# Performance work log

Measured on AMD Instinct MI355X. Metric: run time of the kernel, lower is better.

Reference implementation:

```python
import jax, jax.numpy as jnp
import numpy as np

B, N, E, H = 2, 4096, 512, 8
D = E // H  # head size


def setup_inputs() -> dict:
    key = jax.random.key(0)
    ks = jax.random.split(key, 11)
    s = 1.0 / np.sqrt(E)
    inp = {
        'q': jax.random.normal(ks[0], (B, N, E), jnp.float32),
        'k': jax.random.normal(ks[1], (B, N, E), jnp.float32),
        'v': jax.random.normal(ks[2], (B, N, E), jnp.float32),
        'Wq': jax.random.uniform(ks[3], (E, E), jnp.float32, -s, s),
        'bq': jax.random.uniform(ks[4], (E,), jnp.float32, -s, s),
        'Wk': jax.random.uniform(ks[5], (E, E), jnp.float32, -s, s),
        'bk': jax.random.uniform(ks[6], (E,), jnp.float32, -s, s),
        'Wv': jax.random.uniform(ks[7], (E, E), jnp.float32, -s, s),
        'bv': jax.random.uniform(ks[8], (E,), jnp.float32, -s, s),
        'Wo': jax.random.uniform(ks[9], (E, E), jnp.float32, -s, s),
        'bo': jax.random.uniform(ks[10], (E,), jnp.float32, -s, s),
    }
    return inp


def reference(q, k, v, Wq, bq, Wk, bk, Wv, bv, Wo, bo):
    # Linear projections (torch Linear: x @ W.T + b)
    qp = (q @ Wq.T + bq).reshape(B, N, H, D).transpose(0, 2, 1, 3)  # [B,H,N,D]
    kp = (k @ Wk.T + bk).reshape(B, N, H, D).transpose(0, 2, 1, 3)
    vp = (v @ Wv.T + bv).reshape(B, N, H, D).transpose(0, 2, 1, 3)
    scores = jnp.einsum('bhnd,bhmd->bhnm', qp, kp) / jnp.sqrt(jnp.float32(D))
    attn = jax.nn.softmax(scores, axis=-1)
    out = jnp.einsum('bhnm,bhmd->bhnd', attn, vp)  # [B,H,N,D]
    out = out.transpose(0, 2, 1, 3).reshape(B, N, E)
    return out @ Wo.T + bo
```

## Files before the change

### kernel.cpp

```cpp
#include <hip/hip_runtime.h>
#include <hip/hip_bf16.h>
#include <cstddef>


typedef __bf16 bf16_t;
typedef __bf16 bf16x8 __attribute__((ext_vector_type(8)));
typedef __bf16 bf16x4 __attribute__((ext_vector_type(4)));
typedef float  f32x4  __attribute__((ext_vector_type(4)));

#define MFMA_BF16 __builtin_amdgcn_mfma_f32_16x16x32_bf16

static __device__ __forceinline__ bf16x8 cvt2(const float4& a, const float4& b) {
  return bf16x8{(bf16_t)a.x,(bf16_t)a.y,(bf16_t)a.z,(bf16_t)a.w,
                (bf16_t)b.x,(bf16_t)b.y,(bf16_t)b.z,(bf16_t)b.w};
}

__global__ void __launch_bounds__(256, 2)
qkv_proj(const float* __restrict__ q, const float* __restrict__ k,
         const float* __restrict__ v,
         const float* __restrict__ Wq, const float* __restrict__ bq,
         const float* __restrict__ Wk, const float* __restrict__ bk,
         const float* __restrict__ Wv, const float* __restrict__ bv,
         bf16_t* __restrict__ Qp, bf16_t* __restrict__ Kp,
         bf16_t* __restrict__ Vt, float qscale)
{
  __shared__ __align__(16) bf16_t As[2][128 * 72];
  __shared__ __align__(16) bf16_t Bs[2][64 * 72];
  const int l     = blockIdx.x;
  const int slice = l >> 9;
  const int inner = l & 511;
  const int mtile = ((inner >> 6) << 3) | (inner & 7);
  const int ntile = (inner >> 3) & 7;
  const int tid   = threadIdx.x;
  const int w     = tid >> 6;
  const int lane  = tid & 63;
  const int lr    = lane & 15;
  const int quad  = lane >> 4;
  const int wm    = w & 1;
  const int wn    = w >> 1;
  const int xrow  = tid >> 1, xcol = (tid & 1) << 5;
  const int wrow  = tid >> 2, wcol = (tid & 3) << 4;

  const float* Xf   = (slice == 0) ? q  : (slice == 1) ? k  : v;
  const float* W    = (slice == 0) ? Wq : (slice == 1) ? Wk : Wv;
  const float* bias = (slice == 0) ? bq : (slice == 1) ? bk : bv;
  const float scale = (slice == 0) ? qscale : 1.0f;

  float bvv[2];
#pragma unroll
  for (int ci = 0; ci < 2; ++ci) bvv[ci] = bias[ntile * 64 + wn * 32 + ci * 16 + lr];

  f32x4 acc[4][2] = {};
  float4 xa[8], wa[4];

#pragma unroll
  for (int j = 0; j < 4; ++j) {
    const float* p = Xf + (size_t)(mtile * 128 + xrow) * 512 + xcol + j * 8;
    xa[2*j]   = *(const float4*)p;
    xa[2*j+1] = *(const float4*)(p + 4);
  }
#pragma unroll
  for (int j = 0; j < 2; ++j) {
    const float* pw = W + (size_t)(ntile * 64 + wrow) * 512 + wcol + j * 8;
    wa[2*j]   = *(const float4*)pw;
    wa[2*j+1] = *(const float4*)(pw + 4);
  }
#pragma unroll
  for (int j = 0; j < 4; ++j)
    *(bf16x8*)(&As[0][xrow * 72 + xcol + j * 8]) = cvt2(xa[2*j], xa[2*j+1]);
#pragma unroll
  for (int j = 0; j < 2; ++j)
    *(bf16x8*)(&Bs[0][wrow * 72 + wcol + j * 8]) = cvt2(wa[2*j], wa[2*j+1]);
  __syncthreads();

  for (int it = 0; it < 8; ++it) {
    const int cur = it & 1, nxt = cur ^ 1;
    if (it != 7) {
      const int k0 = (it + 1) << 6;
#pragma unroll
      for (int j = 0; j < 4; ++j) {
        const float* p = Xf + (size_t)(mtile * 128 + xrow) * 512 + k0 + xcol + j * 8;
        xa[2*j]   = *(const float4*)p;
        xa[2*j+1] = *(const float4*)(p + 4);
      }
#pragma unroll
      for (int j = 0; j < 2; ++j) {
        const float* pw = W + (size_t)(ntile * 64 + wrow) * 512 + k0 + wcol + j * 8;
        wa[2*j]   = *(const float4*)pw;
        wa[2*j+1] = *(const float4*)(pw + 4);
      }
    }
    bf16x8 af[4][2], bfr[2][2];
#pragma unroll
    for (int mi = 0; mi < 4; ++mi)
#pragma unroll
      for (int kh = 0; kh < 2; ++kh)
        af[mi][kh] = *(const bf16x8*)(&As[cur][(wm * 64 + mi * 16 + lr) * 72 + (kh * 4 + quad) * 8]);
#pragma unroll
    for (int ci = 0; ci < 2; ++ci)
#pragma unroll
      for (int kh = 0; kh < 2; ++kh)
        bfr[ci][kh] = *(const bf16x8*)(&Bs[cur][(wn * 32 + ci * 16 + lr) * 72 + (kh * 4 + quad) * 8]);
#pragma unroll
    for (int mi = 0; mi < 4; ++mi)
#pragma unroll
      for (int ci = 0; ci < 2; ++ci) {
        acc[mi][ci] = MFMA_BF16(af[mi][0], bfr[ci][0], acc[mi][ci], 0, 0, 0);
        acc[mi][ci] = MFMA_BF16(af[mi][1], bfr[ci][1], acc[mi][ci], 0, 0, 0);
      }
    if (it != 7) {
#pragma unroll
      for (int j = 0; j < 4; ++j)
        *(bf16x8*)(&As[nxt][xrow * 72 + xcol + j * 8]) = cvt2(xa[2*j], xa[2*j+1]);
#pragma unroll
      for (int j = 0; j < 2; ++j)
        *(bf16x8*)(&Bs[nxt][wrow * 72 + wcol + j * 8]) = cvt2(wa[2*j], wa[2*j+1]);
    }
    __syncthreads();
  }

  bf16_t* outQK = (slice == 0) ? Qp : Kp;
#pragma unroll
  for (int mi = 0; mi < 4; ++mi) {
    const int gm0 = mtile * 128 + wm * 64 + mi * 16 + quad * 4;
#pragma unroll
    for (int ci = 0; ci < 2; ++ci) {
      const int gc = ntile * 64 + wn * 32 + ci * 16 + lr;
      const int h = gc >> 6, dd = gc & 63;
      if (slice < 2) {
#pragma unroll
        for (int r = 0; r < 4; ++r) {
          const int gm = gm0 + r;
          const int b = gm >> 12, n = gm & 4095;
          outQK[(size_t)((b * 8 + h) * 4096 + n) * 64 + dd] =
              (bf16_t)((acc[mi][ci][r] + bvv[ci]) * scale);
        }
      } else {
        const int b = gm0 >> 12, n0 = gm0 & 4095;
        bf16x4 pk;
#pragma unroll
        for (int r = 0; r < 4; ++r) pk[r] = (bf16_t)(acc[mi][ci][r] + bvv[ci]);
        *(bf16x4*)(Vt + (size_t)((b * 8 + h) * 64 + dd) * 4096 + n0) = pk;
      }
    }
  }
}

__global__ void __launch_bounds__(256, 2)
o_proj(const bf16_t* __restrict__ Xb, const float* __restrict__ W,
       const float* __restrict__ bias, float* __restrict__ out)
{
  __shared__ __align__(16) bf16_t As[2][128 * 72];
  __shared__ __align__(16) bf16_t Bs[2][64 * 72];
  const int l     = blockIdx.x;
  const int mtile = ((l >> 6) << 3) | (l & 7);
  const int ntile = (l >> 3) & 7;
  const int tid   = threadIdx.x;
  const int w     = tid >> 6;
  const int lane  = tid & 63;
  const int lr    = lane & 15;
  const int quad  = lane >> 4;
  const int wm    = w & 1;
  const int wn    = w >> 1;
  const int xrow  = tid >> 1, xcol = (tid & 1) << 5;
  const int wrow  = tid >> 2, wcol = (tid & 3) << 4;

  float bvv[2];
#pragma unroll
  for (int ci = 0; ci < 2; ++ci) bvv[ci] = bias[ntile * 64 + wn * 32 + ci * 16 + lr];

  f32x4 acc[4][2] = {};
  float4 wa[4];
  bf16x8 xb[4];

#pragma unroll
  for (int j = 0; j < 4; ++j)
    xb[j] = *(const bf16x8*)(Xb + (size_t)(mtile * 128 + xrow) * 512 + xcol + j * 8);
#pragma unroll
  for (int j = 0; j < 2; ++j) {
    const float* pw = W + (size_t)(ntile * 64 + wrow) * 512 + wcol + j * 8;
    wa[2*j]   = *(const float4*)pw;
    wa[2*j+1] = *(const float4*)(pw + 4);
  }
#pragma unroll
  for (int j = 0; j < 4; ++j)
    *(bf16x8*)(&As[0][xrow * 72 + xcol + j * 8]) = xb[j];
#pragma unroll
  for (int j = 0; j < 2; ++j)
    *(bf16x8*)(&Bs[0][wrow * 72 + wcol + j * 8]) = cvt2(wa[2*j], wa[2*j+1]);
  __syncthreads();

  for (int it = 0; it < 8; ++it) {
    const int cur = it & 1, nxt = cur ^ 1;
    if (it != 7) {
      const int k0 = (it + 1) << 6;
#pragma unroll
      for (int j = 0; j < 4; ++j)
        xb[j] = *(const bf16x8*)(Xb + (size_t)(mtile * 128 + xrow) * 512 + k0 + xcol + j * 8);
#pragma unroll
      for (int j = 0; j < 2; ++j) {
        const float* pw = W + (size_t)(ntile * 64 + wrow) * 512 + k0 + wcol + j * 8;
        wa[2*j]   = *(const float4*)pw;
        wa[2*j+1] = *(const float4*)(pw + 4);
      }
    }
    bf16x8 af[4][2], bfr[2][2];
#pragma unroll
    for (int mi = 0; mi < 4; ++mi)
#pragma unroll
      for (int kh = 0; kh < 2; ++kh)
        af[mi][kh] = *(const bf16x8*)(&As[cur][(wm * 64 + mi * 16 + lr) * 72 + (kh * 4 + quad) * 8]);
#pragma unroll
    for (int ci = 0; ci < 2; ++ci)
#pragma unroll
      for (int kh = 0; kh < 2; ++kh)
        bfr[ci][kh] = *(const bf16x8*)(&Bs[cur][(wn * 32 + ci * 16 + lr) * 72 + (kh * 4 + quad) * 8]);
#pragma unroll
    for (int mi = 0; mi < 4; ++mi)
#pragma unroll
      for (int ci = 0; ci < 2; ++ci) {
        acc[mi][ci] = MFMA_BF16(af[mi][0], bfr[ci][0], acc[mi][ci], 0, 0, 0);
        acc[mi][ci] = MFMA_BF16(af[mi][1], bfr[ci][1], acc[mi][ci], 0, 0, 0);
      }
    if (it != 7) {
#pragma unroll
      for (int j = 0; j < 4; ++j)
        *(bf16x8*)(&As[nxt][xrow * 72 + xcol + j * 8]) = xb[j];
#pragma unroll
      for (int j = 0; j < 2; ++j)
        *(bf16x8*)(&Bs[nxt][wrow * 72 + wcol + j * 8]) = cvt2(wa[2*j], wa[2*j+1]);
    }
    __syncthreads();
  }

#pragma unroll
  for (int mi = 0; mi < 4; ++mi) {
    const int gm0 = mtile * 128 + wm * 64 + mi * 16 + quad * 4;
#pragma unroll
    for (int ci = 0; ci < 2; ++ci) {
      const int gc = ntile * 64 + wn * 32 + ci * 16 + lr;
#pragma unroll
      for (int r = 0; r < 4; ++r)
        out[(size_t)(gm0 + r) * 512 + gc] = acc[mi][ci][r] + bvv[ci];
    }
  }
}

__global__ void __launch_bounds__(256, 2)
flash_attn(const bf16_t* __restrict__ Qp, const bf16_t* __restrict__ Kp,
           const bf16_t* __restrict__ Vt, bf16_t* __restrict__ Oc)
{
  __shared__ __align__(16) bf16_t Klds[2][64 * 72];
  __shared__ __align__(16) bf16_t Vlds[2][64 * 72];
  __shared__ __align__(16) bf16_t Pl[4][32 * 72];

  const int tid  = threadIdx.x;
  const int w    = tid >> 6;
  const int lane = tid & 63, lr = lane & 15, quad = lane >> 4;
  const int bh   = blockIdx.x;
  const int qt0  = blockIdx.y * 128 + w * 32;

  const bf16_t* Qh = Qp + (size_t)bh * 4096 * 64;
  const bf16_t* Kh = Kp + (size_t)bh * 4096 * 64;
  const bf16_t* Vh = Vt + (size_t)bh * 64 * 4096;

  const int srow = w * 16 + (lane >> 2);
  const int scol = (lane & 3) << 4;

  bf16x8 qf[2][2];
#pragma unroll
  for (int qi = 0; qi < 2; ++qi)
#pragma unroll
    for (int kh = 0; kh < 2; ++kh)
      qf[qi][kh] = *(const bf16x8*)(Qh + (size_t)(qt0 + qi * 16 + lr) * 64 + kh * 32 + quad * 8);

  bf16x8 kst[2], vst[2];
#pragma unroll
  for (int j = 0; j < 2; ++j) {
    kst[j] = *(const bf16x8*)(Kh + (size_t)srow * 64 + scol + j * 8);
    vst[j] = *(const bf16x8*)(Vh + (size_t)srow * 4096 + scol + j * 8);
  }
#pragma unroll
  for (int j = 0; j < 2; ++j) {
    *(bf16x8*)(&Klds[0][srow * 72 + scol + j * 8]) = kst[j];
    *(bf16x8*)(&Vlds[0][srow * 72 + scol + j * 8]) = vst[j];
  }
  __syncthreads();

  f32x4 acc[2][4] = {};
  float lsum[2] = {0.f, 0.f};
  const f32x4 zero = {0.f, 0.f, 0.f, 0.f};
  bf16_t* Pw = &Pl[w][0];

  for (int it = 0; it < 64; ++it) {
    const int cur = it & 1, nxt = cur ^ 1;

    if (it != 63) {
      const int kvn = (it + 1) << 6;
#pragma unroll
      for (int j = 0; j < 2; ++j) {
        kst[j] = *(const bf16x8*)(Kh + (size_t)(kvn + srow) * 64 + scol + j * 8);
        vst[j] = *(const bf16x8*)(Vh + (size_t)srow * 4096 + kvn + scol + j * 8);
      }
    }

    bf16x8 kf[4][2];
#pragma unroll
    for (int mt = 0; mt < 4; ++mt)
#pragma unroll
      for (int kh = 0; kh < 2; ++kh)
        kf[mt][kh] = *(const bf16x8*)(&Klds[cur][(mt * 16 + lr) * 72 + (kh * 4 + quad) * 8]);
    bf16x8 vf[4][2];
#pragma unroll
    for (int t = 0; t < 4; ++t)
#pragma unroll
      for (int kvh = 0; kvh < 2; ++kvh)
        vf[t][kvh] = *(const bf16x8*)(&Vlds[cur][(t * 16 + lr) * 72 + (kvh * 4 + quad) * 8]);

    f32x4 sT[4][2];
#pragma unroll
    for (int mt = 0; mt < 4; ++mt)
#pragma unroll
      for (int qi = 0; qi < 2; ++qi) {
        sT[mt][qi] = MFMA_BF16(kf[mt][0], qf[qi][0], zero, 0, 0, 0);
        sT[mt][qi] = MFMA_BF16(kf[mt][1], qf[qi][1], sT[mt][qi], 0, 0, 0);
      }

#pragma unroll
    for (int mt = 0; mt < 4; ++mt)
#pragma unroll
      for (int qi = 0; qi < 2; ++qi) {
        float p0 = __builtin_amdgcn_exp2f(sT[mt][qi][0]);
        float p1 = __builtin_amdgcn_exp2f(sT[mt][qi][1]);
        float p2 = __builtin_amdgcn_exp2f(sT[mt][qi][2]);
        float p3 = __builtin_amdgcn_exp2f(sT[mt][qi][3]);
        lsum[qi] += (p0 + p1) + (p2 + p3);
        bf16x4 pk = {(bf16_t)p0, (bf16_t)p1, (bf16_t)p2, (bf16_t)p3};
        *(bf16x4*)(Pw + (qi * 16 + lr) * 72 + mt * 16 + quad * 4) = pk;
      }

    bf16x8 pa[2][2];
#pragma unroll
    for (int qi = 0; qi < 2; ++qi)
#pragma unroll
      for (int kvh = 0; kvh < 2; ++kvh)
        pa[qi][kvh] = *(const bf16x8*)(Pw + (qi * 16 + lr) * 72 + kvh * 32 + quad * 8);

#pragma unroll
    for (int t = 0; t < 4; ++t)
#pragma unroll
      for (int qi = 0; qi < 2; ++qi) {
        acc[qi][t] = MFMA_BF16(pa[qi][0], vf[t][0], acc[qi][t], 0, 0, 0);
        acc[qi][t] = MFMA_BF16(pa[qi][1], vf[t][1], acc[qi][t], 0, 0, 0);
      }

    if (it != 63) {
#pragma unroll
      for (int j = 0; j < 2; ++j) {
        *(bf16x8*)(&Klds[nxt][srow * 72 + scol + j * 8]) = kst[j];
        *(bf16x8*)(&Vlds[nxt][srow * 72 + scol + j * 8]) = vst[j];
      }
    }
    __syncthreads();
  }

#pragma unroll
  for (int qi = 0; qi < 2; ++qi) {
    lsum[qi] += __shfl_xor(lsum[qi], 16);
    lsum[qi] += __shfl_xor(lsum[qi], 32);
  }

  const int b = bh >> 3, h = bh & 7;
  bf16_t* Ob = Oc + (size_t)b * 4096 * 512 + h * 64;
#pragma unroll
  for (int qi = 0; qi < 2; ++qi) {
    float inv[4];
#pragma unroll
    for (int r = 0; r < 4; ++r)
      inv[r] = 1.0f / __shfl(lsum[qi], quad * 4 + r);
#pragma unroll
    for (int t = 0; t < 4; ++t)
#pragma unroll
      for (int r = 0; r < 4; ++r) {
        const int n = qt0 + qi * 16 + quad * 4 + r;
        Ob[(size_t)n * 512 + t * 16 + lr] = (bf16_t)(acc[qi][t][r] * inv[r]);
      }
  }
}

extern "C" void kernel_launch(void* const* d_in, const int* in_sizes, int n_in,
                              void* d_out, int out_size, void* d_ws, size_t ws_size,
                              hipStream_t stream)
{
  const float* q  = (const float*)d_in[0];
  const float* k  = (const float*)d_in[1];
  const float* v  = (const float*)d_in[2];
  const float* Wq = (const float*)d_in[3];
  const float* bq = (const float*)d_in[4];
  const float* Wk = (const float*)d_in[5];
  const float* bk = (const float*)d_in[6];
  const float* Wv = (const float*)d_in[7];
  const float* bv = (const float*)d_in[8];
  const float* Wo = (const float*)d_in[9];
  const float* bo = (const float*)d_in[10];

  const size_t HEAD_ELEMS = (size_t)2 * 8 * 4096 * 64;
  bf16_t* Qp = (bf16_t*)d_ws;
  bf16_t* Kp = Qp + HEAD_ELEMS;
  bf16_t* Vt = Kp + HEAD_ELEMS;
  bf16_t* Oc = Vt + HEAD_ELEMS;

  const float qscale = 0.125f * 1.44269504f;

  qkv_proj<<<dim3(1536), 256, 0, stream>>>(q, k, v, Wq, bq, Wk, bk, Wv, bv,
                                           Qp, Kp, Vt, qscale);
  flash_attn<<<dim3(16, 32), 256, 0, stream>>>(Qp, Kp, Vt, Oc);
  o_proj<<<dim3(512), 256, 0, stream>>>(Oc, Wo, bo, (float*)d_out);
}
```

Measured before the change: 268.6 us.

## Widen projection GEMM tiles to 128x128 and pass P via register permlane swaps

The QKV and output projection GEMMs move from 128x64 to 128x128 output tiles, which halves the block count and doubles each block's MFMA work per LDS load, so fp32 X tiles are re-read and converted less often. In flash attention, the exp'd probability tile is no longer written to and read back from a per-wave LDS buffer. It is instead packed with v_cvt_pk_bf16_f32 and reshuffled into the MFMA A-operand layout with v_permlane32/16_swap. The larger tiles raise register and LDS use and give fewer blocks for occupancy. The permlane path relies on a specific lane-mapping assumption that must match the MFMA layout.

New measurement: 260.6 us. 1.03x faster.

```diff
diff --git a/kernel.cpp b/kernel.cpp
--- a/kernel.cpp
+++ b/kernel.cpp
@@ -1,6 +1,7 @@
 #include <hip/hip_runtime.h>
 #include <hip/hip_bf16.h>
 #include <cstddef>
+#include <cstdint>
 
 
 typedef __bf16 bf16_t;
@@ -13,6 +14,12 @@
 static __device__ __forceinline__ bf16x8 cvt2(const float4& a, const float4& b) {
   return bf16x8{(bf16_t)a.x,(bf16_t)a.y,(bf16_t)a.z,(bf16_t)a.w,
                 (bf16_t)b.x,(bf16_t)b.y,(bf16_t)b.z,(bf16_t)b.w};
+}
+
+static __device__ __forceinline__ uint32_t pk2(float a, float b) {
+  uint32_t r;
+  asm("v_cvt_pk_bf16_f32 %0, %1, %2" : "=v"(r) : "v"(a), "v"(b));
+  return r;
 }
 
 __global__ void __launch_bounds__(256, 2)
@@ -25,12 +32,12 @@
          bf16_t* __restrict__ Vt, float qscale)
 {
   __shared__ __align__(16) bf16_t As[2][128 * 72];
-  __shared__ __align__(16) bf16_t Bs[2][64 * 72];
+  __shared__ __align__(16) bf16_t Bs[2][128 * 72];
   const int l     = blockIdx.x;
-  const int slice = l >> 9;
-  const int inner = l & 511;
-  const int mtile = ((inner >> 6) << 3) | (inner & 7);
-  const int ntile = (inner >> 3) & 7;
+  const int slice = l >> 8;
+  const int inner = l & 255;
+  const int mtile = ((inner >> 5) << 3) | (inner & 7);
+  const int ntile = (inner >> 3) & 3;
   const int tid   = threadIdx.x;
   const int w     = tid >> 6;
   const int lane  = tid & 63;
@@ -39,38 +46,33 @@
   const int wm    = w & 1;
   const int wn    = w >> 1;
   const int xrow  = tid >> 1, xcol = (tid & 1) << 5;
-  const int wrow  = tid >> 2, wcol = (tid & 3) << 4;
 
   const float* Xf   = (slice == 0) ? q  : (slice == 1) ? k  : v;
   const float* W    = (slice == 0) ? Wq : (slice == 1) ? Wk : Wv;
   const float* bias = (slice == 0) ? bq : (slice == 1) ? bk : bv;
   const float scale = (slice == 0) ? qscale : 1.0f;
 
-  float bvv[2];
-#pragma unroll
-  for (int ci = 0; ci < 2; ++ci) bvv[ci] = bias[ntile * 64 + wn * 32 + ci * 16 + lr];
-
-  f32x4 acc[4][2] = {};
-  float4 xa[8], wa[4];
+  float bvv[4];
+#pragma unroll
+  for (int ci = 0; ci < 4; ++ci) bvv[ci] = bias[ntile * 128 + wn * 64 + ci * 16 + lr];
+
+  f32x4 acc[4][4] = {};
+  float4 xa[8], wa[8];
 
 #pragma unroll
   for (int j = 0; j < 4; ++j) {
     const float* p = Xf + (size_t)(mtile * 128 + xrow) * 512 + xcol + j * 8;
     xa[2*j]   = *(const float4*)p;
     xa[2*j+1] = *(const float4*)(p + 4);
-  }
-#pragma unroll
-  for (int j = 0; j < 2; ++j) {
-    const float* pw = W + (size_t)(ntile * 64 + wrow) * 512 + wcol + j * 8;
+    const float* pw = W + (size_t)(ntile * 128 + xrow) * 512 + xcol + j * 8;
     wa[2*j]   = *(const float4*)pw;
     wa[2*j+1] = *(const float4*)(pw + 4);
   }
 #pragma unroll
-  for (int j = 0; j < 4; ++j)
+  for (int j = 0; j < 4; ++j) {
     *(bf16x8*)(&As[0][xrow * 72 + xcol + j * 8]) = cvt2(xa[2*j], xa[2*j+1]);
-#pragma unroll
-  for (int j = 0; j < 2; ++j)
-    *(bf16x8*)(&Bs[0][wrow * 72 + wcol + j * 8]) = cvt2(wa[2*j], wa[2*j+1]);
+    *(bf16x8*)(&Bs[0][xrow * 72 + xcol + j * 8]) = cvt2(wa[2*j], wa[2*j+1]);
+  }
   __syncthreads();
 
   for (int it = 0; it < 8; ++it) {
@@ -82,39 +84,35 @@
         const float* p = Xf + (size_t)(mtile * 128 + xrow) * 512 + k0 + xcol + j * 8;
         xa[2*j]   = *(const float4*)p;
         xa[2*j+1] = *(const float4*)(p + 4);
-      }
-#pragma unroll
-      for (int j = 0; j < 2; ++j) {
-        const float* pw = W + (size_t)(ntile * 64 + wrow) * 512 + k0 + wcol + j * 8;
+        const float* pw = W + (size_t)(ntile * 128 + xrow) * 512 + k0 + xcol + j * 8;
         wa[2*j]   = *(const float4*)pw;
         wa[2*j+1] = *(const float4*)(pw + 4);
       }
     }
-    bf16x8 af[4][2], bfr[2][2];
+    bf16x8 af[4][2], bfr[4][2];
 #pragma unroll
     for (int mi = 0; mi < 4; ++mi)
 #pragma unroll
       for (int kh = 0; kh < 2; ++kh)
         af[mi][kh] = *(const bf16x8*)(&As[cur][(wm * 64 + mi * 16 + lr) * 72 + (kh * 4 + quad) * 8]);
 #pragma unroll
-    for (int ci = 0; ci < 2; ++ci)
+    for (int ci = 0; ci < 4; ++ci)
 #pragma unroll
       for (int kh = 0; kh < 2; ++kh)
-        bfr[ci][kh] = *(const bf16x8*)(&Bs[cur][(wn * 32 + ci * 16 + lr) * 72 + (kh * 4 + quad) * 8]);
+        bfr[ci][kh] = *(const bf16x8*)(&Bs[cur][(wn * 64 + ci * 16 + lr) * 72 + (kh * 4 + quad) * 8]);
 #pragma unroll
     for (int mi = 0; mi < 4; ++mi)
 #pragma unroll
-      for (int ci = 0; ci < 2; ++ci) {
+      for (int ci = 0; ci < 4; ++ci) {
         acc[mi][ci] = MFMA_BF16(af[mi][0], bfr[ci][0], acc[mi][ci], 0, 0, 0);
         acc[mi][ci] = MFMA_BF16(af[mi][1], bfr[ci][1], acc[mi][ci], 0, 0, 0);
       }
     if (it != 7) {
 #pragma unroll
-      for (int j = 0; j < 4; ++j)
+      for (int j = 0; j < 4; ++j) {
         *(bf16x8*)(&As[nxt][xrow * 72 + xcol + j * 8]) = cvt2(xa[2*j], xa[2*j+1]);
-#pragma unroll
-      for (int j = 0; j < 2; ++j)
-        *(bf16x8*)(&Bs[nxt][wrow * 72 + wcol + j * 8]) = cvt2(wa[2*j], wa[2*j+1]);
+        *(bf16x8*)(&Bs[nxt][xrow * 72 + xcol + j * 8]) = cvt2(wa[2*j], wa[2*j+1]);
+      }
     }
     __syncthreads();
   }
@@ -124,8 +122,8 @@
   for (int mi = 0; mi < 4; ++mi) {
     const int gm0 = mtile * 128 + wm * 64 + mi * 16 + quad * 4;
 #pragma unroll
-    for (int ci = 0; ci < 2; ++ci) {
-      const int gc = ntile * 64 + wn * 32 + ci * 16 + lr;
+    for (int ci = 0; ci < 4; ++ci) {
+      const int gc = ntile * 128 + wn * 64 + ci * 16 + lr;
       const int h = gc >> 6, dd = gc & 63;
       if (slice < 2) {
 #pragma unroll
@@ -151,10 +149,10 @@
        const float* __restrict__ bias, float* __restrict__ out)
 {
   __shared__ __align__(16) bf16_t As[2][128 * 72];
-  __shared__ __align__(16) bf16_t Bs[2][64 * 72];
+  __shared__ __align__(16) bf16_t Bs[2][128 * 72];
   const int l     = blockIdx.x;
-  const int mtile = ((l >> 6) << 3) | (l & 7);
-  const int ntile = (l >> 3) & 7;
+  const int mtile = ((l >> 5) << 3) | (l & 7);
+  const int ntile = (l >> 3) & 3;
   const int tid   = threadIdx.x;
   const int w     = tid >> 6;
   const int lane  = tid & 63;
@@ -163,31 +161,27 @@
   const int wm    = w & 1;
   const int wn    = w >> 1;
   const int xrow  = tid >> 1, xcol = (tid & 1) << 5;
-  const int wrow  = tid >> 2, wcol = (tid & 3) << 4;
-
-  float bvv[2];
-#pragma unroll
-  for (int ci = 0; ci < 2; ++ci) bvv[ci] = bias[ntile * 64 + wn * 32 + ci * 16 + lr];
-
-  f32x4 acc[4][2] = {};
-  float4 wa[4];
+
+  float bvv[4];
+#pragma unroll
+  for (int ci = 0; ci < 4; ++ci) bvv[ci] = bias[ntile * 128 + wn * 64 + ci * 16 + lr];
+
+  f32x4 acc[4][4] = {};
+  float4 wa[8];
   bf16x8 xb[4];
 
 #pragma unroll
-  for (int j = 0; j < 4; ++j)
+  for (int j = 0; j < 4; ++j) {
     xb[j] = *(const bf16x8*)(Xb + (size_t)(mtile * 128 + xrow) * 512 + xcol + j * 8);
-#pragma unroll
-  for (int j = 0; j < 2; ++j) {
-    const float* pw = W + (size_t)(ntile * 64 + wrow) * 512 + wcol + j * 8;
+    const float* pw = W + (size_t)(ntile * 128 + xrow) * 512 + xcol + j * 8;
     wa[2*j]   = *(const float4*)pw;
     wa[2*j+1] = *(const float4*)(pw + 4);
   }
 #pragma unroll
-  for (int j = 0; j < 4; ++j)
+  for (int j = 0; j < 4; ++j) {
     *(bf16x8*)(&As[0][xrow * 72 + xcol + j * 8]) = xb[j];
-#pragma unroll
-  for (int j = 0; j < 2; ++j)
-    *(bf16x8*)(&Bs[0][wrow * 72 + wcol + j * 8]) = cvt2(wa[2*j], wa[2*j+1]);
+    *(bf16x8*)(&Bs[0][xrow * 72 + xcol + j * 8]) = cvt2(wa[2*j], wa[2*j+1]);
+  }
   __syncthreads();
 
   for (int it = 0; it < 8; ++it) {
@@ -195,40 +189,37 @@
     if (it != 7) {
       const int k0 = (it + 1) << 6;
 #pragma unroll
-      for (int j = 0; j < 4; ++j)
+      for (int j = 0; j < 4; ++j) {
         xb[j] = *(const bf16x8*)(Xb + (size_t)(mtile * 128 + xrow) * 512 + k0 + xcol + j * 8);
-#pragma unroll
-      for (int j = 0; j < 2; ++j) {
-        const float* pw = W + (size_t)(ntile * 64 + wrow) * 512 + k0 + wcol + j * 8;
+        const float* pw = W + (size_t)(ntile * 128 + xrow) * 512 + k0 + xcol + j * 8;
         wa[2*j]   = *(const float4*)pw;
         wa[2*j+1] = *(const float4*)(pw + 4);
       }
     }
-    bf16x8 af[4][2], bfr[2][2];
+    bf16x8 af[4][2], bfr[4][2];
 #pragma unroll
     for (int mi = 0; mi < 4; ++mi)
 #pragma unroll
       for (int kh = 0; kh < 2; ++kh)
         af[mi][kh] = *(const bf16x8*)(&As[cur][(wm * 64 + mi * 16 + lr) * 72 + (kh * 4 + quad) * 8]);
 #pragma unroll
-    for (int ci = 0; ci < 2; ++ci)
+    for (int ci = 0; ci < 4; ++ci)
 #pragma unroll
       for (int kh = 0; kh < 2; ++kh)
-        bfr[ci][kh] = *(const bf16x8*)(&Bs[cur][(wn * 32 + ci * 16 + lr) * 72 + (kh * 4 + quad) * 8]);
+        bfr[ci][kh] = *(const bf16x8*)(&Bs[cur][(wn * 64 + ci * 16 + lr) * 72 + (kh * 4 + quad) * 8]);
 #pragma unroll
     for (int mi = 0; mi < 4; ++mi)
 #pragma unroll
-      for (int ci = 0; ci < 2; ++ci) {
+      for (int ci = 0; ci < 4; ++ci) {
         acc[mi][ci] = MFMA_BF16(af[mi][0], bfr[ci][0], acc[mi][ci], 0, 0, 0);
         acc[mi][ci] = MFMA_BF16(af[mi][1], bfr[ci][1], acc[mi][ci], 0, 0, 0);
       }
     if (it != 7) {
 #pragma unroll
-      for (int j = 0; j < 4; ++j)
+      for (int j = 0; j < 4; ++j) {
         *(bf16x8*)(&As[nxt][xrow * 72 + xcol + j * 8]) = xb[j];
-#pragma unroll
-      for (int j = 0; j < 2; ++j)
-        *(bf16x8*)(&Bs[nxt][wrow * 72 + wcol + j * 8]) = cvt2(wa[2*j], wa[2*j+1]);
+        *(bf16x8*)(&Bs[nxt][xrow * 72 + xcol + j * 8]) = cvt2(wa[2*j], wa[2*j+1]);
+      }
     }
     __syncthreads();
   }
@@ -237,8 +228,8 @@
   for (int mi = 0; mi < 4; ++mi) {
     const int gm0 = mtile * 128 + wm * 64 + mi * 16 + quad * 4;
 #pragma unroll
-    for (int ci = 0; ci < 2; ++ci) {
-      const int gc = ntile * 64 + wn * 32 + ci * 16 + lr;
+    for (int ci = 0; ci < 4; ++ci) {
+      const int gc = ntile * 128 + wn * 64 + ci * 16 + lr;
 #pragma unroll
       for (int r = 0; r < 4; ++r)
         out[(size_t)(gm0 + r) * 512 + gc] = acc[mi][ci][r] + bvv[ci];
@@ -252,7 +243,6 @@
 {
   __shared__ __align__(16) bf16_t Klds[2][64 * 72];
   __shared__ __align__(16) bf16_t Vlds[2][64 * 72];
-  __shared__ __align__(16) bf16_t Pl[4][32 * 72];
 
   const int tid  = threadIdx.x;
   const int w    = tid >> 6;
@@ -290,7 +280,6 @@
   f32x4 acc[2][4] = {};
   float lsum[2] = {0.f, 0.f};
   const f32x4 zero = {0.f, 0.f, 0.f, 0.f};
-  bf16_t* Pw = &Pl[w][0];
 
   for (int it = 0; it < 64; ++it) {
     const int cur = it & 1, nxt = cur ^ 1;
@@ -326,25 +315,33 @@
         sT[mt][qi] = MFMA_BF16(kf[mt][1], qf[qi][1], sT[mt][qi], 0, 0, 0);
       }
 
-#pragma unroll
-    for (int mt = 0; mt < 4; ++mt)
-#pragma unroll
-      for (int qi = 0; qi < 2; ++qi) {
+    bf16x8 pa[2][2];
+#pragma unroll
+    for (int qi = 0; qi < 2; ++qi) {
+      uint32_t ap[4], bp[4];
+#pragma unroll
+      for (int mt = 0; mt < 4; ++mt) {
         float p0 = __builtin_amdgcn_exp2f(sT[mt][qi][0]);
         float p1 = __builtin_amdgcn_exp2f(sT[mt][qi][1]);
         float p2 = __builtin_amdgcn_exp2f(sT[mt][qi][2]);
         float p3 = __builtin_amdgcn_exp2f(sT[mt][qi][3]);
         lsum[qi] += (p0 + p1) + (p2 + p3);
-        bf16x4 pk = {(bf16_t)p0, (bf16_t)p1, (bf16_t)p2, (bf16_t)p3};
-        *(bf16x4*)(Pw + (qi * 16 + lr) * 72 + mt * 16 + quad * 4) = pk;
-      }
-
-    bf16x8 pa[2][2];
-#pragma unroll
-    for (int qi = 0; qi < 2; ++qi)
-#pragma unroll
-      for (int kvh = 0; kvh < 2; ++kvh)
-        pa[qi][kvh] = *(const bf16x8*)(Pw + (qi * 16 + lr) * 72 + kvh * 32 + quad * 8);
+        ap[mt] = pk2(p0, p1);
+        bp[mt] = pk2(p2, p3);
+      }
+#pragma unroll
+      for (int kvh = 0; kvh < 2; ++kvh) {
+        uint32_t xa_ = ap[2 * kvh], ya_ = ap[2 * kvh + 1];
+        asm("v_permlane32_swap_b32 %0, %1" : "+v"(xa_), "+v"(ya_));
+        asm("v_permlane16_swap_b32 %0, %1" : "+v"(xa_), "+v"(ya_));
+        uint32_t xb_ = bp[2 * kvh], yb_ = bp[2 * kvh + 1];
+        asm("v_permlane32_swap_b32 %0, %1" : "+v"(xb_), "+v"(yb_));
+        asm("v_permlane16_swap_b32 %0, %1" : "+v"(xb_), "+v"(yb_));
+        union { uint32_t u[4]; bf16x8 v; } pu;
+        pu.u[0] = xa_; pu.u[1] = xb_; pu.u[2] = ya_; pu.u[3] = yb_;
+        pa[qi][kvh] = pu.v;
+      }
+    }
 
 #pragma unroll
     for (int t = 0; t < 4; ++t)
@@ -412,8 +409,8 @@
 
   const float qscale = 0.125f * 1.44269504f;
 
-  qkv_proj<<<dim3(1536), 256, 0, stream>>>(q, k, v, Wq, bq, Wk, bk, Wv, bv,
-                                           Qp, Kp, Vt, qscale);
+  qkv_proj<<<dim3(768), 256, 0, stream>>>(q, k, v, Wq, bq, Wk, bk, Wv, bv,
+                                          Qp, Kp, Vt, qscale);
   flash_attn<<<dim3(16, 32), 256, 0, stream>>>(Qp, Kp, Vt, Oc);
-  o_proj<<<dim3(512), 256, 0, stream>>>(Oc, Wo, bo, (float*)d_out);
-}
+  o_proj<<<dim3(256), 256, 0, stream>>>(Oc, Wo, bo, (float*)d_out);
+}
```
